# Performance work log

Hardware: AMD Instinct MI355X
Metric: run time of the kernel (lower is better)

## Reference

```python
import jax, jax.numpy as jnp
import numpy as np

D_MODEL = 2048
N_EXPERTS = 64
N_TOK = 16384
THRESH = 0.9   # confidence_threshold


def setup_inputs() -> dict:
    key = jax.random.key(0)
    k1, k2 = jax.random.split(key, 2)
    x = jax.random.normal(k1, (N_TOK, D_MODEL), dtype=jnp.float32)
    W = jax.random.normal(k2, (D_MODEL, N_EXPERTS), dtype=jnp.float32) * (1.0 / np.sqrt(D_MODEL))
    b = jnp.zeros((N_EXPERTS,), dtype=jnp.float32)
    return {"x": x, "W": W, "b": b}


def reference(x, W, b):
    # gate + softmax over experts
    logits = x @ W + b                                  # [N, E]
    probs = jax.nn.softmax(logits, axis=-1)
    # descending sort along expert axis
    order = jnp.argsort(-probs, axis=-1)                # [N, E] int
    sorted_probs = jnp.take_along_axis(probs, order, axis=-1)
    # nucleus-style cutoff: experts whose preceding cumulative mass < threshold
    cum = jnp.cumsum(sorted_probs, axis=-1)
    shifted_cumsum = cum - sorted_probs
    is_active = shifted_cumsum < THRESH
    is_active = is_active.at[..., 0].set(True)          # always keep top-1
    active_probs = sorted_probs * is_active.astype(sorted_probs.dtype)
    total_mass = active_probs.sum(axis=-1, keepdims=True)
    active_weights = active_probs / (total_mass + 1e-6)
    # scatter back to original expert order == gather with inverse permutation
    inv_order = jnp.argsort(order, axis=-1)
    routing_weights = jnp.take_along_axis(active_weights, inv_order, axis=-1)
    active_count = is_active.sum(axis=-1)
    return routing_weights, probs, active_count
```

## Files before the change

### kernel.cpp

```cpp
#include <hip/hip_runtime.h>

#define D_MODEL   2048
#define N_EXPERTS 64
#define THRESH    0.9f
#define TOK_BLK   16
#define KV_WAVES  16

typedef __attribute__((ext_vector_type(8))) short bf16x8;
typedef __attribute__((ext_vector_type(4))) float f32x4;

union FragU { unsigned u[4]; bf16x8 v; };

__device__ __forceinline__ unsigned pack_hi(float f0, float f1) {
    return __builtin_amdgcn_perm(__float_as_uint(f1), __float_as_uint(f0), 0x07060302u);
}
__device__ __forceinline__ float trunc_bf(float f) {
    return __uint_as_float(__float_as_uint(f) & 0xFFFF0000u);
}

__global__ void prepack_w(const float* __restrict__ W,
                          bf16x8* __restrict__ c0, bf16x8* __restrict__ c1,
                          bf16x8* __restrict__ c2)
{
    const int ks = blockIdx.x;
    const int nt = threadIdx.x >> 6;
    const int l  = threadIdx.x & 63;
    const int col  = nt * 16 + (l & 15);
    const int krow = ks * 32 + ((l >> 4) << 3);
    FragU F0, F1, F2;
#pragma unroll
    for (int j = 0; j < 4; ++j) {
        const float a = W[(size_t)(krow + 2*j    ) * N_EXPERTS + col];
        const float b = W[(size_t)(krow + 2*j + 1) * N_EXPERTS + col];
        const float ra = a - trunc_bf(a),  rb = b - trunc_bf(b);
        const float sa = ra - trunc_bf(ra), sb = rb - trunc_bf(rb);
        F0.u[j] = pack_hi(a,  b);
        F1.u[j] = pack_hi(ra, rb);
        F2.u[j] = pack_hi(sa, sb);
    }
    const int idx = (ks * 4 + nt) * 64 + l;
    c0[idx] = F0.v; c1[idx] = F1.v; c2[idx] = F2.v;
}

__global__ __launch_bounds__(1024, 8)
void dynk_mfma(const float* __restrict__ x,
               const bf16x8* __restrict__ c0, const bf16x8* __restrict__ c1,
               const bf16x8* __restrict__ c2,
               const float* __restrict__ b,
               float* __restrict__ out_rw, float* __restrict__ out_probs,
               float* __restrict__ out_cnt, int n_tok)
{
    __shared__ float red[KV_WAVES * 16 * 64];
    const int l  = threadIdx.x & 63;
    const int kv = threadIdx.x >> 6;
    const int tok0 = blockIdx.x * TOK_BLK;

    const int r = l & 15;
    const int q = l >> 4;
    int xr = tok0 + r; if (xr >= n_tok) xr = n_tok - 1;
    const float* xrow = x + (size_t)xr * D_MODEL + q * 8;

    f32x4 acc[4] = {f32x4{0,0,0,0}, f32x4{0,0,0,0}, f32x4{0,0,0,0}, f32x4{0,0,0,0}};

#pragma unroll
    for (int s = 0; s < 4; ++s) {
        const int ks = kv * 4 + s;
        const float4 xa = *reinterpret_cast<const float4*>(xrow + ks * 32);
        const float4 xb = *reinterpret_cast<const float4*>(xrow + ks * 32 + 4);
        const float f[8] = {xa.x, xa.y, xa.z, xa.w, xb.x, xb.y, xb.z, xb.w};

        FragU A0, A1, A2;
#pragma unroll
        for (int j = 0; j < 4; ++j) {
            const float p0 = f[2*j], p1 = f[2*j+1];
            const float r0 = p0 - trunc_bf(p0), r1 = p1 - trunc_bf(p1);
            const float s0 = r0 - trunc_bf(r0), s1 = r1 - trunc_bf(r1);
            A0.u[j] = pack_hi(p0, p1);
            A1.u[j] = pack_hi(r0, r1);
            A2.u[j] = pack_hi(s0, s1);
        }

#pragma unroll
        for (int nt = 0; nt < 4; ++nt) {
            const int idx = (ks * 4 + nt) * 64 + l;
            const bf16x8 B0 = c0[idx];
            const bf16x8 B1 = c1[idx];
            const bf16x8 B2 = c2[idx];
            acc[nt] = __builtin_amdgcn_mfma_f32_16x16x32_bf16(A2.v, B0, acc[nt], 0, 0, 0);
            acc[nt] = __builtin_amdgcn_mfma_f32_16x16x32_bf16(A0.v, B2, acc[nt], 0, 0, 0);
            acc[nt] = __builtin_amdgcn_mfma_f32_16x16x32_bf16(A1.v, B1, acc[nt], 0, 0, 0);
            acc[nt] = __builtin_amdgcn_mfma_f32_16x16x32_bf16(A1.v, B0, acc[nt], 0, 0, 0);
            acc[nt] = __builtin_amdgcn_mfma_f32_16x16x32_bf16(A0.v, B1, acc[nt], 0, 0, 0);
            acc[nt] = __builtin_amdgcn_mfma_f32_16x16x32_bf16(A0.v, B0, acc[nt], 0, 0, 0);
        }
    }

#pragma unroll
    for (int nt = 0; nt < 4; ++nt)
#pragma unroll
        for (int j = 0; j < 4; ++j)
            red[(kv * 16 + q * 4 + j) * 64 + (nt * 16 + r)] = acc[nt][j];
    __syncthreads();

    const long tok = (long)tok0 + kv;
    if (tok < n_tok) {
        float lg = b[l];
#pragma unroll
        for (int kk = 0; kk < KV_WAVES; ++kk) lg += red[(kk * 16 + kv) * 64 + l];

        float m = lg;
#pragma unroll
        for (int d = 32; d > 0; d >>= 1) m = fmaxf(m, __shfl_xor(m, d));
        const float e = expf(lg - m);
        float sden = e;
#pragma unroll
        for (int d = 32; d > 0; d >>= 1) sden += __shfl_xor(sden, d);
        const float p = e / sden;

        float S = 0.f;
#pragma unroll
        for (int j = 0; j < 64; ++j) {
            const float pj = __shfl(p, j);
            const bool before = (pj > p) || (pj == p && j < l);
            S += before ? pj : 0.f;
        }
        const bool active = (S < THRESH);

        float total = active ? p : 0.f;
#pragma unroll
        for (int d = 32; d > 0; d >>= 1) total += __shfl_xor(total, d);

        const int cnt = __popcll(__ballot(active));
        const float wgt = active ? p / (total + 1e-6f) : 0.f;

        out_rw[tok * N_EXPERTS + l]    = wgt;
        out_probs[tok * N_EXPERTS + l] = p;
        if (l == 0) out_cnt[tok] = (float)cnt;
    }
}

__global__ __launch_bounds__(256, 2)
void dynk_fallback(const float* __restrict__ x, const float* __restrict__ W,
                   const float* __restrict__ b, float* __restrict__ out_rw,
                   float* __restrict__ out_probs, float* __restrict__ out_cnt,
                   int n_tok)
{
    const int lane = threadIdx.x & 63;
    const int wid  = threadIdx.x >> 6;
    const long tok0 = (long)blockIdx.x * 32 + (long)wid * 8;
    if (tok0 >= n_tok) return;
    float acc[8];
    const float bias = b[lane];
#pragma unroll
    for (int t = 0; t < 8; ++t) acc[t] = bias;
    const float* xp = x + tok0 * D_MODEL;
    for (int k0 = 0; k0 < D_MODEL; k0 += 8) {
        float w[8];
#pragma unroll
        for (int j = 0; j < 8; ++j) w[j] = W[(long)(k0 + j) * N_EXPERTS + lane];
#pragma unroll
        for (int t = 0; t < 8; ++t) {
            const float4 xa = *reinterpret_cast<const float4*>(xp + (long)t * D_MODEL + k0);
            const float4 xb = *reinterpret_cast<const float4*>(xp + (long)t * D_MODEL + k0 + 4);
            acc[t] = fmaf(xa.x, w[0], acc[t]); acc[t] = fmaf(xa.y, w[1], acc[t]);
            acc[t] = fmaf(xa.z, w[2], acc[t]); acc[t] = fmaf(xa.w, w[3], acc[t]);
            acc[t] = fmaf(xb.x, w[4], acc[t]); acc[t] = fmaf(xb.y, w[5], acc[t]);
            acc[t] = fmaf(xb.z, w[6], acc[t]); acc[t] = fmaf(xb.w, w[7], acc[t]);
        }
    }
#pragma unroll 1
    for (int t = 0; t < 8; ++t) {
        const long tok = tok0 + t;
        const float lgt = acc[t];
        float m = lgt;
#pragma unroll
        for (int d = 32; d > 0; d >>= 1) m = fmaxf(m, __shfl_xor(m, d));
        const float e = expf(lgt - m);
        float s = e;
#pragma unroll
        for (int d = 32; d > 0; d >>= 1) s += __shfl_xor(s, d);
        const float p = e / s;
        float S = 0.f;
#pragma unroll
        for (int j = 0; j < 64; ++j) {
            const float pj = __shfl(p, j);
            S += ((pj > p) || (pj == p && j < lane)) ? pj : 0.f;
        }
        const bool active = (S < THRESH);
        float total = active ? p : 0.f;
#pragma unroll
        for (int d = 32; d > 0; d >>= 1) total += __shfl_xor(total, d);
        const int cnt = __popcll(__ballot(active));
        const float wgt = active ? p / (total + 1e-6f) : 0.f;
        out_rw[tok * N_EXPERTS + lane]    = wgt;
        out_probs[tok * N_EXPERTS + lane] = p;
        if (lane == 0) out_cnt[tok] = (float)cnt;
    }
}

extern "C" void kernel_launch(void* const* d_in, const int* in_sizes, int n_in,
                              void* d_out, int out_size, void* d_ws, size_t ws_size,
                              hipStream_t stream) {
    const float* x = (const float*)d_in[0];
    const float* W = (const float*)d_in[1];
    const float* b = (const float*)d_in[2];
    const int n_tok = in_sizes[0] / D_MODEL;

    float* out   = (float*)d_out;
    float* rw    = out;
    float* probs = out + (size_t)n_tok * N_EXPERTS;
    float* cnt   = out + 2 * (size_t)n_tok * N_EXPERTS;

    const size_t frag_elems = 64 * 4 * 64;
    const size_t need = 3 * frag_elems * sizeof(bf16x8);

    if (ws_size < need) {
        const int blocks = (n_tok + 31) / 32;
        dynk_fallback<<<blocks, 256, 0, stream>>>(x, W, b, rw, probs, cnt, n_tok);
        return;
    }

    bf16x8* c0 = (bf16x8*)d_ws;
    bf16x8* c1 = c0 + frag_elems;
    bf16x8* c2 = c1 + frag_elems;

    prepack_w<<<64, 256, 0, stream>>>(W, c0, c1, c2);

    const int blocks = (n_tok + TOK_BLK - 1) / TOK_BLK;
    dynk_mfma<<<blocks, 1024, 0, stream>>>(x, c0, c1, c2, b, rw, probs, cnt, n_tok);
}
```

Before: 224.1 us.

## Restructure MFMA gate kernel to 32-token blocks with 4-way K split

Each block now handles 32 tokens with 8 waves: two 16-token row groups, each split four ways along K, so each wave covers 512 of the K dimension instead of 128. Cross-wave reduction work and shared-memory traffic per token shrink, and each wave runs a longer MFMA loop. Each wave then runs the softmax/top-p epilogue for four tokens sequentially. The packed weight fragments are now reloaded by two row groups per block rather than one, and per-CU occupancy changes with the new 512-thread launch bounds.

```diff
diff --git a/kernel.cpp b/kernel.cpp
--- a/kernel.cpp
+++ b/kernel.cpp
@@ -3,8 +3,9 @@
 #define D_MODEL   2048
 #define N_EXPERTS 64
 #define THRESH    0.9f
-#define TOK_BLK   16
-#define KV_WAVES  16
+#define TOK_BLK   32
+#define NWAVES    8
+#define KSPLIT    4
 
 typedef __attribute__((ext_vector_type(8))) short bf16x8;
 typedef __attribute__((ext_vector_type(4))) float f32x4;
@@ -42,7 +43,7 @@
     c0[idx] = F0.v; c1[idx] = F1.v; c2[idx] = F2.v;
 }
 
-__global__ __launch_bounds__(1024, 8)
+__global__ __launch_bounds__(512, 6)
 void dynk_mfma(const float* __restrict__ x,
                const bf16x8* __restrict__ c0, const bf16x8* __restrict__ c1,
                const bf16x8* __restrict__ c2,
@@ -50,23 +51,29 @@
                float* __restrict__ out_rw, float* __restrict__ out_probs,
                float* __restrict__ out_cnt, int n_tok)
 {
-    __shared__ float red[KV_WAVES * 16 * 64];
+    __shared__ float red[NWAVES * 16 * 64];
     const int l  = threadIdx.x & 63;
-    const int kv = threadIdx.x >> 6;
+    const int w  = threadIdx.x >> 6;
+    const int t  = w >> 2;
+    const int kv = w & 3;
     const int tok0 = blockIdx.x * TOK_BLK;
 
     const int r = l & 15;
     const int q = l >> 4;
-    int xr = tok0 + r; if (xr >= n_tok) xr = n_tok - 1;
-    const float* xrow = x + (size_t)xr * D_MODEL + q * 8;
+    int xr = tok0 + t * 16 + r; if (xr >= n_tok) xr = n_tok - 1;
+    const float* xrow = x + (size_t)xr * D_MODEL + kv * 512 + q * 8;
+
+    const size_t bbase = (size_t)(kv * 16 * 4) * 64 + l;
+    const bf16x8* B0p = c0 + bbase;
+    const bf16x8* B1p = c1 + bbase;
+    const bf16x8* B2p = c2 + bbase;
 
     f32x4 acc[4] = {f32x4{0,0,0,0}, f32x4{0,0,0,0}, f32x4{0,0,0,0}, f32x4{0,0,0,0}};
 
-#pragma unroll
-    for (int s = 0; s < 4; ++s) {
-        const int ks = kv * 4 + s;
-        const float4 xa = *reinterpret_cast<const float4*>(xrow + ks * 32);
-        const float4 xb = *reinterpret_cast<const float4*>(xrow + ks * 32 + 4);
+#pragma unroll 4
+    for (int s = 0; s < 16; ++s) {
+        const float4 xa = *reinterpret_cast<const float4*>(xrow + s * 32);
+        const float4 xb = *reinterpret_cast<const float4*>(xrow + s * 32 + 4);
         const float f[8] = {xa.x, xa.y, xa.z, xa.w, xb.x, xb.y, xb.z, xb.w};
 
         FragU A0, A1, A2;
@@ -82,10 +89,10 @@
 
 #pragma unroll
         for (int nt = 0; nt < 4; ++nt) {
-            const int idx = (ks * 4 + nt) * 64 + l;
-            const bf16x8 B0 = c0[idx];
-            const bf16x8 B1 = c1[idx];
-            const bf16x8 B2 = c2[idx];
+            const int off = s * 256 + nt * 64;
+            const bf16x8 B0 = B0p[off];
+            const bf16x8 B1 = B1p[off];
+            const bf16x8 B2 = B2p[off];
             acc[nt] = __builtin_amdgcn_mfma_f32_16x16x32_bf16(A2.v, B0, acc[nt], 0, 0, 0);
             acc[nt] = __builtin_amdgcn_mfma_f32_16x16x32_bf16(A0.v, B2, acc[nt], 0, 0, 0);
             acc[nt] = __builtin_amdgcn_mfma_f32_16x16x32_bf16(A1.v, B1, acc[nt], 0, 0, 0);
@@ -99,23 +106,30 @@
     for (int nt = 0; nt < 4; ++nt)
 #pragma unroll
         for (int j = 0; j < 4; ++j)
-            red[(kv * 16 + q * 4 + j) * 64 + (nt * 16 + r)] = acc[nt][j];
+            red[(w * 16 + q * 4 + j) * 64 + (nt * 16 + r)] = acc[nt][j];
     __syncthreads();
 
-    const long tok = (long)tok0 + kv;
-    if (tok < n_tok) {
+#pragma unroll 1
+    for (int e = 0; e < 4; ++e) {
+        const int tt  = w * 4 + e;
+        const int t2  = tt >> 4;
+        const int row = tt & 15;
+        const long tok = (long)tok0 + tt;
+        if (tok >= n_tok) break;
+
         float lg = b[l];
 #pragma unroll
-        for (int kk = 0; kk < KV_WAVES; ++kk) lg += red[(kk * 16 + kv) * 64 + l];
+        for (int k2 = 0; k2 < KSPLIT; ++k2)
+            lg += red[((t2 * 4 + k2) * 16 + row) * 64 + l];
 
         float m = lg;
 #pragma unroll
         for (int d = 32; d > 0; d >>= 1) m = fmaxf(m, __shfl_xor(m, d));
-        const float e = expf(lg - m);
-        float sden = e;
+        const float e0 = expf(lg - m);
+        float sden = e0;
 #pragma unroll
         for (int d = 32; d > 0; d >>= 1) sden += __shfl_xor(sden, d);
-        const float p = e / sden;
+        const float p = e0 / sden;
 
         float S = 0.f;
 #pragma unroll
@@ -227,5 +241,5 @@
     prepack_w<<<64, 256, 0, stream>>>(W, c0, c1, c2);
 
     const int blocks = (n_tok + TOK_BLK - 1) / TOK_BLK;
-    dynk_mfma<<<blocks, 1024, 0, stream>>>(x, c0, c1, c2, b, rw, probs, cnt, n_tok);
-}
+    dynk_mfma<<<blocks, 512, 0, stream>>>(x, c0, c1, c2, b, rw, probs, cnt, n_tok);
+}
```

Result: slower. 237.2 us (+5.9%).
